# Kernel tuning notes

Hardware: AMD Instinct MI355X
Metric: run time of the kernel (lower is better)

The kernel has to match this reference:

```python
import jax, jax.numpy as jnp
import numpy as np

B, S, D, H = 2, 2048, 1024, 16
DH = D // H  # d_head = 64
EPS = 1e-6


def _rms_norm(x, eps=EPS):
    # norm_without_weight: RMS normalization over last dim, no learned scale
    return x * jax.lax.rsqrt(jnp.mean(x * x, axis=-1, keepdims=True) + eps)


def _rope_tables(seq_len, dim):
    # angular_freq: dim//4 geometric freqs + dim//4 zeros -> dim//2 total
    freqs = (1.0 / 1024.0) ** jnp.linspace(0.0, 1.0, dim // 4, dtype=jnp.float32)
    freqs = jnp.concatenate([freqs, jnp.zeros((dim // 4,), dtype=jnp.float32)])
    theta = jnp.outer(jnp.arange(seq_len, dtype=jnp.float32), freqs)  # [S, dim//2]
    return jnp.cos(theta), jnp.sin(theta)


def _apply_rope(x_bhsk, cos, sin):
    # x: [B,H,S,DH]; cos/sin: [S, DH//2] broadcast over batch/heads
    c = cos[None, None, :, :]
    s = sin[None, None, :, :]
    xf = x_bhsk.astype(jnp.float32)
    x1, x2 = jnp.split(xf, 2, axis=-1)
    y1 = x1 * c + x2 * s
    y2 = -x1 * s + x2 * c
    return jnp.concatenate([y1, y2], axis=-1).astype(x_bhsk.dtype)


def setup_inputs() -> dict:
    key = jax.random.key(0)
    k0, k1, k2, k3, k4 = jax.random.split(key, 5)
    scale = 1.0 / np.sqrt(D)
    x = jax.random.normal(k0, (B, S, D), dtype=jnp.float32)
    # equinox Linear stores weight as [out_features, in_features], y = x @ W.T
    w_q = jax.random.normal(k1, (D, D), dtype=jnp.float32) * scale
    w_k = jax.random.normal(k2, (D, D), dtype=jnp.float32) * scale
    w_v = jax.random.normal(k3, (D, D), dtype=jnp.float32) * scale
    w_o = jax.random.normal(k4, (D, D), dtype=jnp.float32) * scale
    mask = jnp.tril(jnp.ones((S, S), dtype=bool))  # causal
    return {"x": x, "w_q": w_q, "w_k": w_k, "w_v": w_v, "w_o": w_o, "mask": mask}


def reference(x, w_q, w_k, w_v, w_o, mask):
    b, s, d = x.shape
    # projections (no bias); [B,S,D] @ [D,D].T -> [B,S,D] -> [B,H,S,DH]
    def proj(w):
        y = jnp.einsum('bsd,ed->bse', x, w)
        return y.reshape(b, s, H, DH).transpose(0, 2, 1, 3)
    q, k, v = proj(w_q), proj(w_k), proj(w_v)
    # QK-norm (RMS, no weight)
    q = _rms_norm(q)
    k = _rms_norm(k)
    # rotary over sequence axis
    cos, sin = _rope_tables(s, DH)
    q = _apply_rope(q, cos, sin)
    k = _apply_rope(k, cos, sin)
    # scores [B,H,S,S]
    scores = jnp.einsum('bhsk,bhtk->bhst', q, k) / jnp.sqrt(jnp.float32(DH))
    scores = jnp.where(mask[None, None, :, :], scores, -jnp.inf)
    weights = jax.nn.softmax(scores, axis=-1)
    out = jnp.einsum('bhst,bhtk->bhsk', weights, v)  # [B,H,S,DH]
    out = out.transpose(0, 2, 1, 3).reshape(b, s, d)
    return jnp.einsum('bsd,ed->bse', out, w_o)
```

## Files before the change

kernel.cpp:

```cpp
#include <hip/hip_runtime.h>
#include <hip/hip_bf16.h>

#define Bb 2
#define Ss 2048
#define Dd 1024
#define Hh 16
#define Tt ((size_t)Bb*Ss*Dd)
#define WNn ((size_t)Dd*Dd)

typedef short bf16x8 __attribute__((ext_vector_type(8)));
typedef short bf16x4 __attribute__((ext_vector_type(4)));
typedef float floatx4 __attribute__((ext_vector_type(4)));
typedef unsigned short u16;

__device__ inline void gld16(void* lds, const void* g) {
  __builtin_amdgcn_global_load_lds(
      (const __attribute__((address_space(1))) unsigned int*)g,
      (__attribute__((address_space(3))) unsigned int*)lds, 16, 0, 0);
}

__device__ inline float bf2f(u16 u) {
  unsigned int x = ((unsigned int)u) << 16;
  float f; __builtin_memcpy(&f, &x, 4); return f;
}
__device__ inline u16 f2bf(float f) {
  unsigned int x; __builtin_memcpy(&x, &f, 4);
  x = (x + 0x7fff + ((x >> 16) & 1)) >> 16;
  return (u16)x;
}
__device__ inline float u2f(unsigned int x) {
  float f; __builtin_memcpy(&f, &x, 4); return f;
}
__device__ inline unsigned int cvtpk(float lo, float hi) {
  unsigned int r;
  asm("v_cvt_pk_bf16_f32 %0, %1, %2" : "=v"(r) : "v"(lo), "v"(hi));
  return r;
}

__global__ void sniff(const unsigned int* __restrict__ x, unsigned int* __restrict__ flag,
                      int nwords) {
  __shared__ int cnt;
  if (threadIdx.x == 0) cnt = 0;
  __syncthreads();
  int local = 0;
  for (int i = threadIdx.x; i < nwords; i += blockDim.x) {
    unsigned int wd = x[i];
    if (((wd >> 7)  & 0xFFu) == 0xFFu) local++;
    if (((wd >> 23) & 0xFFu) == 0xFFu) local++;
  }
  atomicAdd(&cnt, local);
  __syncthreads();
  if (threadIdx.x == 0) *flag = (cnt >= 64) ? 1u : 0u;
}

__global__ __launch_bounds__(256) void convert_all(
    const void* __restrict__ x,  const void* __restrict__ wq,
    const void* __restrict__ wk, const void* __restrict__ wv,
    const void* __restrict__ wo, u16* __restrict__ dst,
    int smode, const unsigned int* __restrict__ flag) {
  const int gb = blockIdx.x;
  const void* src; size_t base; int lb;
  if (gb < 2048)      { src = x;  base = 0;            lb = gb;        }
  else if (gb < 2560) { src = wq; base = Tt;           lb = gb - 2048; }
  else if (gb < 3072) { src = wk; base = Tt + WNn;     lb = gb - 2560; }
  else if (gb < 3584) { src = wv; base = Tt + 2*WNn;   lb = gb - 3072; }
  else                { src = wo; base = Tt + 3*WNn;   lb = gb - 3584; }
  const size_t off = (size_t)lb*2048 + threadIdx.x*8;
  const bool f32 = (smode >= 0) ? (smode == 1) : (*flag != 0u);
  bf16x8 v;
  if (f32) {
    const float* s = (const float*)src + off;
#pragma unroll
    for (int j = 0; j < 8; j++) v[j] = (short)f2bf(s[j]);
  } else {
    v = *(const bf16x8*)((const u16*)src + off);
  }
  *(bf16x8*)(dst + base + off) = v;
}

__global__ __launch_bounds__(256) void gemm_bt(
    const u16* __restrict__ A,
    const u16* __restrict__ W0, const u16* __restrict__ W1, const u16* __restrict__ W2,
    void* __restrict__ C0, void* __restrict__ C1, void* __restrict__ C2,
    int M, int N, int K, const unsigned int* __restrict__ flag, int outMode, int mode)
{
  const u16* W; void* C;
  if (blockIdx.z == 0)      { W = W0; C = C0; }
  else if (blockIdx.z == 1) { W = W1; C = C1; }
  else                      { W = W2; C = C2; }

  __shared__ __align__(16) u16 sA[128*32];
  __shared__ __align__(16) u16 sB[128*32];

  const int tid  = threadIdx.x;
  const int lane = tid & 63;
  const int w    = tid >> 6;
  const int wm = w >> 1, wn = w & 1;
  const int col = lane & 15, quad = lane >> 4;
  const int bm = blockIdx.y, bn = blockIdx.x;

  floatx4 acc[4][4] = {};

  const int c0 = tid, c1 = tid + 256;
  const size_t aOff0 = (size_t)(bm*128 + (c0 >> 2))*K + (c0 & 3)*8;
  const size_t aOff1 = (size_t)(bm*128 + (c1 >> 2))*K + (c1 & 3)*8;
  const size_t bOff0 = (size_t)(bn*128 + (c0 >> 2))*K + (c0 & 3)*8;
  const size_t bOff1 = (size_t)(bn*128 + (c1 >> 2))*K + (c1 & 3)*8;

  for (int kk = 0; kk < K; kk += 32) {
    gld16(&sA[c0*8], A + aOff0 + kk);
    gld16(&sA[c1*8], A + aOff1 + kk);
    gld16(&sB[c0*8], W + bOff0 + kk);
    gld16(&sB[c1*8], W + bOff1 + kk);
    __syncthreads();
    bf16x8 af[4], bfr[4];
#pragma unroll
    for (int i = 0; i < 4; i++)
      af[i] = *(const bf16x8*)&sA[(wm*64 + i*16 + col)*32 + quad*8];
#pragma unroll
    for (int j = 0; j < 4; j++)
      bfr[j] = *(const bf16x8*)&sB[(wn*64 + j*16 + col)*32 + quad*8];
#pragma unroll
    for (int i = 0; i < 4; i++)
#pragma unroll
      for (int j = 0; j < 4; j++)
        acc[i][j] = __builtin_amdgcn_mfma_f32_16x16x32_bf16(af[i], bfr[j], acc[i][j], 0, 0, 0);
    __syncthreads();
  }

  if (mode == 0 && blockIdx.z == 2) {
    u16* Ct = (u16*)C;
#pragma unroll
    for (int i = 0; i < 4; i++)
#pragma unroll
      for (int j = 0; j < 4; j++) {
        int d = bn*128 + wn*64 + j*16 + col;
        int g = bm*128 + wm*64 + i*16 + quad*4;
        int hh = d >> 6, dl = d & 63;
        int bb = g >> 11, s = g & (Ss - 1);
        bf16x4 pk;
#pragma unroll
        for (int r = 0; r < 4; r++) pk[r] = (short)f2bf(acc[i][j][r]);
        *(bf16x4*)&Ct[((size_t)(bb*Hh + hh)*64 + dl)*Ss + s] = pk;
      }
  } else if (mode == 0) {
    const float qs = (blockIdx.z == 0) ? 0.125f : 1.0f;
    const float freq = exp2f((-10.0f/15.0f) * (float)col);
    u16* Co = (u16*)C;
    const size_t cb = (size_t)(bn*128 + wn*64 + col);
#pragma unroll
    for (int i = 0; i < 4; i++)
#pragma unroll
      for (int r = 0; r < 4; r++) {
        float ss = 0.0f;
#pragma unroll
        for (int j = 0; j < 4; j++) ss += acc[i][j][r]*acc[i][j][r];
        ss += __shfl_xor(ss, 1, 64);
        ss += __shfl_xor(ss, 2, 64);
        ss += __shfl_xor(ss, 4, 64);
        ss += __shfl_xor(ss, 8, 64);
        float rn = rsqrtf(ss*(1.0f/64.0f) + 1e-6f) * qs;
        int grow = bm*128 + wm*64 + i*16 + quad*4 + r;
        float th = (float)(grow & (Ss - 1)) * freq;
        float c = cosf(th), sn = sinf(th);
        float x0 = acc[i][0][r]*rn, x1 = acc[i][1][r]*rn;
        float x2 = acc[i][2][r]*rn, x3 = acc[i][3][r]*rn;
        size_t rowb = (size_t)grow*N + cb;
        Co[rowb]      = f2bf(x0*c + x2*sn);
        Co[rowb + 16] = f2bf(x1);
        Co[rowb + 32] = f2bf(x2*c - x0*sn);
        Co[rowb + 48] = f2bf(x3);
      }
  } else {
    const bool f32o = (outMode == 1) || (outMode == -1 && *flag != 0u);
#pragma unroll
    for (int i = 0; i < 4; i++)
#pragma unroll
      for (int j = 0; j < 4; j++)
#pragma unroll
        for (int r = 0; r < 4; r++) {
          int grow = bm*128 + wm*64 + i*16 + quad*4 + r;
          int gcol = bn*128 + wn*64 + j*16 + col;
          size_t idx = (size_t)grow*N + gcol;
          float v = acc[i][j][r];
          if (f32o) ((float*)C)[idx] = v;
          else      ((u16*)C)[idx]   = f2bf(v);
        }
  }
}

__global__ __launch_bounds__(256) void attn(
    const u16* __restrict__ Q, const u16* __restrict__ Kv,
    const u16* __restrict__ Vt, u16* __restrict__ O)
{
  __shared__ __align__(16) u16 sK[2][64*72];
  __shared__ __align__(16) u16 sV[2][2][64*32];
  __shared__ __align__(16) u16 sP[4][16*72];

  const int tid  = threadIdx.x;
  const int lane = tid & 63;
  const int w    = tid >> 6;
  const int col = lane & 15, quad = lane >> 4;
  const int bh = blockIdx.x;
  const int qt = 31 - (int)blockIdx.y;
  const int b = bh >> 4, h = bh & 15;
  const size_t base  = (size_t)b*Ss*Dd + (size_t)h*64;
  const size_t vbase = (size_t)bh*64*Ss;

  const int krow = tid >> 2;
  const int kch  = (tid & 3) * 2;
  const int vrow = tid >> 2;
  const int vcp  = (tid & 3) ^ (vrow & 3) ^ ((vrow >> 2) & 3);
  const u16* Vh = Vt + vbase + (size_t)vrow*Ss + vcp*8;
  const int xorv = quad ^ (col & 3) ^ ((col >> 2) & 3);
  u16* sPw = &sP[w][0];
  const float L2E = 1.44269504f;

  const int q0 = qt * 64;
  const int nk = qt + 1;
  const int qmin = q0 + w*16;

  bf16x8 qf0, qf1;
  {
    const size_t qoff = base + (size_t)(q0 + w*16 + col)*Dd + quad*8;
    qf0 = *(const bf16x8*)(Q + qoff);
    qf1 = *(const bf16x8*)(Q + qoff + 32);
  }
  floatx4 oacc[4] = {};
  float mi[4], li[4];
#pragma unroll
  for (int r = 0; r < 4; r++) { mi[r] = -1e30f; li[r] = 0.0f; }

  {
    const u16* kg = Kv + base + (size_t)krow*Dd + kch*8;
    bf16x8 ka = *(const bf16x8*)kg;
    bf16x8 kb = *(const bf16x8*)(kg + 8);
    gld16(&sV[0][0][tid*8], Vh);
    gld16(&sV[0][1][tid*8], Vh + 32);
    *(bf16x8*)&sK[0][krow*72 + kch*8]     = ka;
    *(bf16x8*)&sK[0][krow*72 + kch*8 + 8] = kb;
    __syncthreads();
  }

  for (int kt = 0; kt < nk; kt++) {
    const int t0 = kt*64;
    const int cur = kt & 1, nxt = cur ^ 1;
    const bool more = (kt + 1 < nk);
    bf16x8 ka, kb;
    if (more) {
      const u16* kg = Kv + base + (size_t)(t0 + 64 + krow)*Dd + kch*8;
      ka = *(const bf16x8*)kg;
      kb = *(const bf16x8*)(kg + 8);
      gld16(&sV[nxt][0][tid*8], Vh + t0 + 64);
      gld16(&sV[nxt][1][tid*8], Vh + t0 + 96);
    }

    floatx4 sc[4] = {};
    __builtin_amdgcn_s_setprio(1);
#pragma unroll
    for (int ts = 0; ts < 4; ts++) {
      bf16x8 k0 = *(const bf16x8*)&sK[cur][(ts*16 + col)*72 + quad*8];
      bf16x8 k1 = *(const bf16x8*)&sK[cur][(ts*16 + col)*72 + 32 + quad*8];
      sc[ts] = __builtin_amdgcn_mfma_f32_16x16x32_bf16(qf0, k0, sc[ts], 0,0,0);
      sc[ts] = __builtin_amdgcn_mfma_f32_16x16x32_bf16(qf1, k1, sc[ts], 0,0,0);
    }
    __builtin_amdgcn_s_setprio(0);

    const bool boundary = (t0 + 63 > qmin);
    float mxr[4];
    float needmax = 0.0f;
#pragma unroll
    for (int r = 0; r < 4; r++) {
      if (boundary) {
        const int qr = q0 + w*16 + quad*4 + r;
        if (t0 +      col > qr) sc[0][r] = -1e30f;
        if (t0 + 16 + col > qr) sc[1][r] = -1e30f;
        if (t0 + 32 + col > qr) sc[2][r] = -1e30f;
        if (t0 + 48 + col > qr) sc[3][r] = -1e30f;
      }
      float mx = fmaxf(fmaxf(sc[0][r], sc[1][r]), fmaxf(sc[2][r], sc[3][r]));
      mx = fmaxf(mx, __shfl_xor(mx, 1, 64));
      mx = fmaxf(mx, __shfl_xor(mx, 2, 64));
      mx = fmaxf(mx, __shfl_xor(mx, 4, 64));
      mx = fmaxf(mx, __shfl_xor(mx, 8, 64));
      mxr[r] = mx;
      needmax = fmaxf(needmax, mx - mi[r]);
    }
    if (!__all(needmax <= 8.0f)) {
      float alr[4];
#pragma unroll
      for (int r = 0; r < 4; r++) {
        float mn = fmaxf(mi[r], mxr[r]);
        float al = exp2f((mi[r] - mn)*L2E);
        mi[r] = mn; li[r] *= al; alr[r] = al;
      }
#pragma unroll
      for (int db = 0; db < 4; db++)
#pragma unroll
        for (int r = 0; r < 4; r++) oacc[db][r] *= alr[r];
    }
#pragma unroll
    for (int r = 0; r < 4; r++) {
      const float nb = -mi[r]*L2E;
      float p0 = exp2f(fmaf(sc[0][r], L2E, nb));
      float p1 = exp2f(fmaf(sc[1][r], L2E, nb));
      float p2 = exp2f(fmaf(sc[2][r], L2E, nb));
      float p3 = exp2f(fmaf(sc[3][r], L2E, nb));
      unsigned int pk01 = cvtpk(p0, p1);
      unsigned int pk23 = cvtpk(p2, p3);
      const int rw = (quad*4 + r)*72;
      sPw[rw + col]      = (u16)pk01;
      sPw[rw + 16 + col] = (u16)(pk01 >> 16);
      sPw[rw + 32 + col] = (u16)pk23;
      sPw[rw + 48 + col] = (u16)(pk23 >> 16);
      li[r] += (u2f(pk01 << 16) + u2f(pk01 & 0xffff0000u))
             + (u2f(pk23 << 16) + u2f(pk23 & 0xffff0000u));
    }
    bf16x8 pa0 = *(const bf16x8*)&sPw[col*72 + quad*8];
    bf16x8 pa1 = *(const bf16x8*)&sPw[col*72 + 32 + quad*8];
    __builtin_amdgcn_s_setprio(1);
#pragma unroll
    for (int db = 0; db < 4; db++) {
      const int vs = (db*16 + col)*32 + xorv*8;
      bf16x8 vb0 = *(const bf16x8*)&sV[cur][0][vs];
      bf16x8 vb1 = *(const bf16x8*)&sV[cur][1][vs];
      oacc[db] = __builtin_amdgcn_mfma_f32_16x16x32_bf16(pa0, vb0, oacc[db], 0,0,0);
      oacc[db] = __builtin_amdgcn_mfma_f32_16x16x32_bf16(pa1, vb1, oacc[db], 0,0,0);
    }
    __builtin_amdgcn_s_setprio(0);

    if (more) {
      *(bf16x8*)&sK[nxt][krow*72 + kch*8]     = ka;
      *(bf16x8*)&sK[nxt][krow*72 + kch*8 + 8] = kb;
    }
    __syncthreads();
  }

  float inv[4];
#pragma unroll
  for (int r = 0; r < 4; r++) {
    float s = li[r];
    s += __shfl_xor(s, 1, 64);
    s += __shfl_xor(s, 2, 64);
    s += __shfl_xor(s, 4, 64);
    s += __shfl_xor(s, 8, 64);
    inv[r] = 1.0f / s;
  }
#pragma unroll
  for (int db = 0; db < 4; db++)
#pragma unroll
    for (int r = 0; r < 4; r++)
      O[base + (size_t)(q0 + w*16 + quad*4 + r)*Dd + db*16 + col] =
          f2bf(oacc[db][r] * inv[r]);
}

extern "C" void kernel_launch(void* const* d_in, const int* in_sizes, int n_in,
                              void* d_out, int out_size, void* d_ws, size_t ws_size,
                              hipStream_t stream) {
  const void* x  = d_in[0];
  const void* wq = d_in[1];
  const void* wk = d_in[2];
  const void* wv = d_in[3];
  const void* wo = d_in[4];

  const size_t T  = Tt;
  const size_t WN = WNn;

  char* ws = (char*)d_ws;
  unsigned int* flag = (unsigned int*)ws;
  u16* xb  = (u16*)(ws + 256);
  u16* wqb = xb  + T;
  u16* wkb = wqb + WN;
  u16* wvb = wkb + WN;
  u16* wob = wvb + WN;
  u16* Qb  = wob + WN;
  u16* Kb  = Qb + T;
  u16* Vb  = Kb + T;
  u16* AO  = Vb + T;

  int smode = -1;
  if (in_sizes && n_in > 0) {
    if (in_sizes[0] == (int)(T*4))      smode = 1;
    else if (in_sizes[0] == (int)(T*2)) smode = 0;
  }
  if (smode < 0)
    sniff<<<1, 1024, 0, stream>>>((const unsigned int*)x, flag, 65536);

  convert_all<<<4096, 256, 0, stream>>>(x, wq, wk, wv, wo, xb, smode, flag);

  gemm_bt<<<dim3(8, 32, 3), 256, 0, stream>>>(xb, wqb, wkb, wvb, Qb, Kb, Vb,
                                              4096, 1024, 1024, flag, 0, 0);
  attn<<<dim3(32, 32), 256, 0, stream>>>(Qb, Kb, Vb, AO);
  gemm_bt<<<dim3(8, 32, 1), 256, 0, stream>>>(AO, wob, wob, wob, d_out, d_out, d_out,
                                              4096, 1024, 1024, flag, smode, 1);
}
```

Before: 265.5 us.

## Process two 64-row query tiles per attention block to reuse K/V tiles

Each attention workgroup now handles 128 query rows, two 64-row sub-tiles per wave, and shares every staged K/V LDS tile between them. The first sub-tile skips key tiles beyond its causal range. This halves K/V global loads and LDS staging per query and halves the grid size. It costs more registers per thread (two sets of accumulators and softmax state), adds a launch-bounds occupancy hint, and leaves fewer, longer blocks, which may hurt load balance across CUs.

```diff
diff --git a/kernel.cpp b/kernel.cpp
--- a/kernel.cpp
+++ b/kernel.cpp
@@ -189,7 +189,7 @@
   }
 }
 
-__global__ __launch_bounds__(256) void attn(
+__global__ __launch_bounds__(256, 3) void attn(
     const u16* __restrict__ Q, const u16* __restrict__ Kv,
     const u16* __restrict__ Vt, u16* __restrict__ O)
 {
@@ -202,7 +202,7 @@
   const int w    = tid >> 6;
   const int col = lane & 15, quad = lane >> 4;
   const int bh = blockIdx.x;
-  const int qt = 31 - (int)blockIdx.y;
+  const int qt = 15 - (int)blockIdx.y;
   const int b = bh >> 4, h = bh & 15;
   const size_t base  = (size_t)b*Ss*Dd + (size_t)h*64;
   const size_t vbase = (size_t)bh*64*Ss;
@@ -216,45 +216,30 @@
   u16* sPw = &sP[w][0];
   const float L2E = 1.44269504f;
 
-  const int q0 = qt * 64;
-  const int nk = qt + 1;
-  const int qmin = q0 + w*16;
-
-  bf16x8 qf0, qf1;
+  const int q0 = qt * 128;
+  const int nk = qt*2 + 2;
+  const int qminA = q0 + w*16;
+  const int qminB = q0 + 64 + w*16;
+
+  bf16x8 qA0, qA1, qB0, qB1;
   {
-    const size_t qoff = base + (size_t)(q0 + w*16 + col)*Dd + quad*8;
-    qf0 = *(const bf16x8*)(Q + qoff);
-    qf1 = *(const bf16x8*)(Q + qoff + 32);
-  }
-  floatx4 oacc[4] = {};
-  float mi[4], li[4];
-#pragma unroll
-  for (int r = 0; r < 4; r++) { mi[r] = -1e30f; li[r] = 0.0f; }
-
-  {
-    const u16* kg = Kv + base + (size_t)krow*Dd + kch*8;
-    bf16x8 ka = *(const bf16x8*)kg;
-    bf16x8 kb = *(const bf16x8*)(kg + 8);
-    gld16(&sV[0][0][tid*8], Vh);
-    gld16(&sV[0][1][tid*8], Vh + 32);
-    *(bf16x8*)&sK[0][krow*72 + kch*8]     = ka;
-    *(bf16x8*)&sK[0][krow*72 + kch*8 + 8] = kb;
-    __syncthreads();
-  }
-
-  for (int kt = 0; kt < nk; kt++) {
-    const int t0 = kt*64;
-    const int cur = kt & 1, nxt = cur ^ 1;
-    const bool more = (kt + 1 < nk);
-    bf16x8 ka, kb;
-    if (more) {
-      const u16* kg = Kv + base + (size_t)(t0 + 64 + krow)*Dd + kch*8;
-      ka = *(const bf16x8*)kg;
-      kb = *(const bf16x8*)(kg + 8);
-      gld16(&sV[nxt][0][tid*8], Vh + t0 + 64);
-      gld16(&sV[nxt][1][tid*8], Vh + t0 + 96);
-    }
-
+    const size_t qoffA = base + (size_t)(qminA + col)*Dd + quad*8;
+    qA0 = *(const bf16x8*)(Q + qoffA);
+    qA1 = *(const bf16x8*)(Q + qoffA + 32);
+    const size_t qoffB = qoffA + (size_t)64*Dd;
+    qB0 = *(const bf16x8*)(Q + qoffB);
+    qB1 = *(const bf16x8*)(Q + qoffB + 32);
+  }
+  floatx4 oaccA[4] = {}, oaccB[4] = {};
+  float miA[4], liA[4], miB[4], liB[4];
+#pragma unroll
+  for (int r = 0; r < 4; r++) {
+    miA[r] = -1e30f; liA[r] = 0.0f;
+    miB[r] = -1e30f; liB[r] = 0.0f;
+  }
+
+  auto process = [&](const bf16x8& qf0, const bf16x8& qf1, floatx4* oacc,
+                     float* mi, float* li, int qmin, int cur, int t0) {
     floatx4 sc[4] = {};
     __builtin_amdgcn_s_setprio(1);
 #pragma unroll
@@ -272,7 +257,7 @@
 #pragma unroll
     for (int r = 0; r < 4; r++) {
       if (boundary) {
-        const int qr = q0 + w*16 + quad*4 + r;
+        const int qr = qmin + quad*4 + r;
         if (t0 +      col > qr) sc[0][r] = -1e30f;
         if (t0 + 16 + col > qr) sc[1][r] = -1e30f;
         if (t0 + 32 + col > qr) sc[2][r] = -1e30f;
@@ -328,6 +313,35 @@
       oacc[db] = __builtin_amdgcn_mfma_f32_16x16x32_bf16(pa1, vb1, oacc[db], 0,0,0);
     }
     __builtin_amdgcn_s_setprio(0);
+  };
+
+  {
+    const u16* kg = Kv + base + (size_t)krow*Dd + kch*8;
+    bf16x8 ka = *(const bf16x8*)kg;
+    bf16x8 kb = *(const bf16x8*)(kg + 8);
+    gld16(&sV[0][0][tid*8], Vh);
+    gld16(&sV[0][1][tid*8], Vh + 32);
+    *(bf16x8*)&sK[0][krow*72 + kch*8]     = ka;
+    *(bf16x8*)&sK[0][krow*72 + kch*8 + 8] = kb;
+    __syncthreads();
+  }
+
+  for (int kt = 0; kt < nk; kt++) {
+    const int t0 = kt*64;
+    const int cur = kt & 1, nxt = cur ^ 1;
+    const bool more = (kt + 1 < nk);
+    bf16x8 ka, kb;
+    if (more) {
+      const u16* kg = Kv + base + (size_t)(t0 + 64 + krow)*Dd + kch*8;
+      ka = *(const bf16x8*)kg;
+      kb = *(const bf16x8*)(kg + 8);
+      gld16(&sV[nxt][0][tid*8], Vh + t0 + 64);
+      gld16(&sV[nxt][1][tid*8], Vh + t0 + 96);
+    }
+
+    if (t0 <= qminA + 15)
+      process(qA0, qA1, oaccA, miA, liA, qminA, cur, t0);
+    process(qB0, qB1, oaccB, miB, liB, qminB, cur, t0);
 
     if (more) {
       *(bf16x8*)&sK[nxt][krow*72 + kch*8]     = ka;
@@ -336,22 +350,30 @@
     __syncthreads();
   }
 
-  float inv[4];
 #pragma unroll
   for (int r = 0; r < 4; r++) {
-    float s = li[r];
-    s += __shfl_xor(s, 1, 64);
-    s += __shfl_xor(s, 2, 64);
-    s += __shfl_xor(s, 4, 64);
-    s += __shfl_xor(s, 8, 64);
-    inv[r] = 1.0f / s;
+    float sA2 = liA[r];
+    sA2 += __shfl_xor(sA2, 1, 64);
+    sA2 += __shfl_xor(sA2, 2, 64);
+    sA2 += __shfl_xor(sA2, 4, 64);
+    sA2 += __shfl_xor(sA2, 8, 64);
+    liA[r] = 1.0f / sA2;
+    float sB2 = liB[r];
+    sB2 += __shfl_xor(sB2, 1, 64);
+    sB2 += __shfl_xor(sB2, 2, 64);
+    sB2 += __shfl_xor(sB2, 4, 64);
+    sB2 += __shfl_xor(sB2, 8, 64);
+    liB[r] = 1.0f / sB2;
   }
 #pragma unroll
   for (int db = 0; db < 4; db++)
 #pragma unroll
-    for (int r = 0; r < 4; r++)
-      O[base + (size_t)(q0 + w*16 + quad*4 + r)*Dd + db*16 + col] =
-          f2bf(oacc[db][r] * inv[r]);
+    for (int r = 0; r < 4; r++) {
+      O[base + (size_t)(qminA + quad*4 + r)*Dd + db*16 + col] =
+          f2bf(oaccA[db][r] * liA[r]);
+      O[base + (size_t)(qminB + quad*4 + r)*Dd + db*16 + col] =
+          f2bf(oaccB[db][r] * liB[r]);
+    }
 }
 
 extern "C" void kernel_launch(void* const* d_in, const int* in_sizes, int n_in,
@@ -390,7 +412,7 @@
 
   gemm_bt<<<dim3(8, 32, 3), 256, 0, stream>>>(xb, wqb, wkb, wvb, Qb, Kb, Vb,
                                               4096, 1024, 1024, flag, 0, 0);
-  attn<<<dim3(32, 32), 256, 0, stream>>>(Qb, Kb, Vb, AO);
+  attn<<<dim3(32, 16), 256, 0, stream>>>(Qb, Kb, Vb, AO);
   gemm_bt<<<dim3(8, 32, 1), 256, 0, stream>>>(AO, wob, wob, wob, d_out, d_out, d_out,
                                               4096, 1024, 1024, flag, smode, 1);
 }
```

After: 300.6 us. 13.2% more time.
